# Kernel optimization log

Hardware: AMD Instinct MI355X
Metric: run time of the kernel (lower is better)

The kernel has to match this reference:

```python
import math
import jax, jax.numpy as jnp
import numpy as np

FACTOR = 2  # init kwarg of AutoCorrelation


def setup_inputs() -> dict:
    key0 = jax.random.key(0)
    kq, kk, kv = jax.random.split(key0, 3)
    B, H, L, D = 8, 8, 2048, 64
    return {
        "query": jax.random.normal(kq, (B, H, L, D), dtype=jnp.float32),
        "key": jax.random.normal(kk, (B, H, L, D), dtype=jnp.float32),
        "value": jax.random.normal(kv, (B, H, L, D), dtype=jnp.float32),
    }


def reference(query, key, value):
    # Inference (eval-mode) path of AutoCorrelation.forward.
    B, H, L, D = query.shape
    L_KV = key.shape[2]
    # _pad_or_truncate_key_value: match key/value length to query length
    if L > L_KV:
        pad = [(0, 0), (0, 0), (0, L - L_KV), (0, 0)]
        key = jnp.pad(key, pad)
        value = jnp.pad(value, pad)
    else:
        key = key[:, :, :L, :]
        value = value[:, :, :L, :]

    # _period_based_dependency: circular cross-correlation via FFT
    qf = jnp.fft.rfft(jnp.swapaxes(query, -2, -1), axis=-1)   # (B,H,D,L//2+1) complex
    kf = jnp.fft.rfft(jnp.swapaxes(key, -2, -1), axis=-1)
    corr = jnp.fft.irfft(qf * jnp.conj(kf), n=L, axis=-1)     # (B,H,D,L)

    # _time_delay_aggregation (eval branch: per-batch topk delays)
    mean_corr = corr.mean(axis=(1, 2))                         # (B,L)
    num_delays = min(FACTOR * math.ceil(math.log(L)), L)
    w, delay_idx = jax.lax.top_k(mean_corr, num_delays)       # (B,k)
    w = jax.nn.softmax(w, axis=-1)

    ar = jnp.arange(L)

    def body(ctx, inp):
        d, wk = inp  # (B,), (B,)
        idx = (ar[None, :] + d[:, None]) % L                   # (B,L) — circular shift == gather from doubled value
        gathered = jnp.take_along_axis(
            value, jnp.broadcast_to(idx[:, None, :, None], value.shape), axis=2
        )                                                      # (B,H,L,D)
        return ctx + wk[:, None, None, None] * gathered, None

    ctx0 = jnp.zeros_like(value)
    context, _ = jax.lax.scan(body, ctx0, (delay_idx.T, w.T))
    return context
```

## Files before the change

### kernel.cpp

```cpp
#include <hip/hip_runtime.h>

static constexpr int LSEQ = 2048;
static constexpr int NB   = 8;
static constexpr int NH   = 8;
static constexpr int ND   = 64;
static constexpr int NDEL = 16;

static constexpr size_t WS_P_OFF     = 0;
static constexpr size_t WS_W_OFF     = 8388608;
static constexpr size_t WS_DELAY_OFF = 8389120;

__device__ __forceinline__ int SWZ(int x) { return x ^ (((x >> 4) & 7) << 1); }

__device__ __forceinline__ int pof(int f) {
    return ((f & 7) << 8) | (((f >> 3) & 7) << 5) | (((f >> 6) & 7) << 2) | (f >> 9);
}
__device__ __forceinline__ int fofp(int p) {
    return (p >> 8) | (((p >> 5) & 7) << 3) | (((p >> 2) & 7) << 6) | ((p & 3) << 9);
}

#define CMUL(ar, ai, br, bi) make_float2((ar)*(br) - (ai)*(bi), (ar)*(bi) + (ai)*(br))

__device__ __forceinline__ void dft8(const float2 x[8], float2 X[8]) {
    const float RH = 0.70710678118654752440f;
    float2 a0 = make_float2(x[0].x + x[4].x, x[0].y + x[4].y);
    float2 a1 = make_float2(x[1].x + x[5].x, x[1].y + x[5].y);
    float2 a2 = make_float2(x[2].x + x[6].x, x[2].y + x[6].y);
    float2 a3 = make_float2(x[3].x + x[7].x, x[3].y + x[7].y);
    float2 b0 = make_float2(x[0].x - x[4].x, x[0].y - x[4].y);
    float  t1r = x[1].x - x[5].x, t1i = x[1].y - x[5].y;
    float2 b1 = make_float2(RH * (t1r + t1i), RH * (t1i - t1r));
    float  t2r = x[2].x - x[6].x, t2i = x[2].y - x[6].y;
    float2 b2 = make_float2(t2i, -t2r);
    float  t3r = x[3].x - x[7].x, t3i = x[3].y - x[7].y;
    float2 b3 = make_float2(RH * (t3i - t3r), -RH * (t3r + t3i));
    float2 c0 = make_float2(a0.x + a2.x, a0.y + a2.y);
    float2 d0 = make_float2(a0.x - a2.x, a0.y - a2.y);
    float2 c1 = make_float2(a1.x + a3.x, a1.y + a3.y);
    float2 d1 = make_float2(a1.y - a3.y, -(a1.x - a3.x));
    X[0] = make_float2(c0.x + c1.x, c0.y + c1.y);
    X[4] = make_float2(c0.x - c1.x, c0.y - c1.y);
    X[2] = make_float2(d0.x + d1.x, d0.y + d1.y);
    X[6] = make_float2(d0.x - d1.x, d0.y - d1.y);
    float2 e0 = make_float2(b0.x + b2.x, b0.y + b2.y);
    float2 f0 = make_float2(b0.x - b2.x, b0.y - b2.y);
    float2 e1 = make_float2(b1.x + b3.x, b1.y + b3.y);
    float2 f1 = make_float2(b1.y - b3.y, -(b1.x - b3.x));
    X[1] = make_float2(e0.x + e1.x, e0.y + e1.y);
    X[5] = make_float2(e0.x - e1.x, e0.y - e1.y);
    X[3] = make_float2(f0.x + f1.x, f0.y + f1.y);
    X[7] = make_float2(f0.x - f1.x, f0.y - f1.y);
}

__device__ __forceinline__ void dft4(const float2 x[4], float2 X[4]) {
    float2 s0 = make_float2(x[0].x + x[2].x, x[0].y + x[2].y);
    float2 s1 = make_float2(x[1].x + x[3].x, x[1].y + x[3].y);
    float2 d0 = make_float2(x[0].x - x[2].x, x[0].y - x[2].y);
    float2 d1 = make_float2(x[1].y - x[3].y, -(x[1].x - x[3].x));
    X[0] = make_float2(s0.x + s1.x, s0.y + s1.y);
    X[2] = make_float2(s0.x - s1.x, s0.y - s1.y);
    X[1] = make_float2(d0.x + d1.x, d0.y + d1.y);
    X[3] = make_float2(d0.x - d1.x, d0.y - d1.y);
}

__device__ __forceinline__ void stageR8(float2* zp, const int adr[8], const float2 W[7]) {
    float2 X[8], Y[8];
    #pragma unroll
    for (int j = 0; j < 8; ++j) X[j] = zp[adr[j]];
    dft8(X, Y);
    #pragma unroll
    for (int m = 1; m < 8; ++m) Y[m] = CMUL(Y[m].x, Y[m].y, W[m-1].x, W[m-1].y);
    #pragma unroll
    for (int m = 0; m < 8; ++m) zp[adr[m]] = Y[m];
}

__device__ __forceinline__ void stageD(float2* zp, const int adr[8], float2 X[8]) {
    float2 xin[8];
    #pragma unroll
    for (int j = 0; j < 8; ++j) xin[j] = zp[adr[j]];
    dft4(&xin[0], &X[0]);
    dft4(&xin[4], &X[4]);
    #pragma unroll
    for (int m = 0; m < 8; ++m) zp[adr[m]] = X[m];
}

__global__ __launch_bounds__(256, 2) void fft_corr(const float* __restrict__ q,
                                                   const float* __restrict__ k,
                                                   float2* __restrict__ Pc) {
    __shared__ float2 z0[LSEQ], z1[LSEQ];
    const int t    = threadIdx.x;
    const int bi   = blockIdx.x;
    const int xcd  = bi & 7;
    const int sl   = bi >> 3;
    const int bh   = xcd * 8 + (sl >> 4);
    const int grp  = (sl >> 1) & 7;
    const int half = sl & 1;
    const int b    = bh >> 3;
    const int h    = bh & 7;
    const size_t base = (size_t)bh * LSEQ * ND + (size_t)(grp * 8 + half * 4);

    float2 WA[7], WB[7], WC[7];
    {
        float sn, cs;
        __sincosf(-6.28318530717958647692f * (float)t / 2048.f, &sn, &cs);
        WA[0] = make_float2(cs, sn);
        __sincosf(-6.28318530717958647692f * (float)(t & 31) / 256.f, &sn, &cs);
        WB[0] = make_float2(cs, sn);
        __sincosf(-6.28318530717958647692f * (float)(t & 3) / 32.f, &sn, &cs);
        WC[0] = make_float2(cs, sn);
        #pragma unroll
        for (int m = 1; m < 7; ++m) {
            WA[m] = CMUL(WA[m-1].x, WA[m-1].y, WA[0].x, WA[0].y);
            WB[m] = CMUL(WB[m-1].x, WB[m-1].y, WB[0].x, WB[0].y);
            WC[m] = CMUL(WC[m-1].x, WC[m-1].y, WC[0].x, WC[0].y);
        }
    }

    int fS[4], pmS[4];
    #pragma unroll
    for (int s = 0; s < 4; ++s) {
        const int cc = (s < 2) ? s : s + 2;
        const int f  = fofp(8 * t + cc);
        const int m  = (2048 - f) & 2047;
        fS[s]  = f;
        pmS[s] = SWZ(pof(m));
    }
    float aFr[4] = {0, 0, 0, 0}, aFi[4] = {0, 0, 0, 0};
    float aS = 0.f;

    const int sbB   = (t >> 5) * 256 + (t & 31);
    const int baseC = (t >> 2) * 32 + (t & 3);
    int adrB[8], adrC[8], adrD[8];
    #pragma unroll
    for (int n = 0; n < 8; ++n) {
        adrB[n] = SWZ(sbB + 32 * n);
        adrC[n] = SWZ(baseC + 4 * n);
        adrD[n] = SWZ(8 * t + n);
    }

    float4 qa[8], ka[8];
    #pragma unroll
    for (int j = 0; j < 8; ++j) {
        const size_t r = base + (size_t)(t + 256 * j) * ND;
        qa[j] = *(const float4*)(q + r);
        ka[j] = *(const float4*)(k + r);
    }
    #pragma unroll
    for (int pr = 0; pr < 2; ++pr) {
        const int c0 = 2 * pr, c1 = 2 * pr + 1;
        float2 X0[8], X1[8], Y0[8], Y1[8];
        #pragma unroll
        for (int j = 0; j < 8; ++j) {
            X0[j] = make_float2((&qa[j].x)[c0], (&ka[j].x)[c0]);
            X1[j] = make_float2((&qa[j].x)[c1], (&ka[j].x)[c1]);
        }
        __syncthreads();

        dft8(X0, Y0);
        dft8(X1, Y1);
        #pragma unroll
        for (int m = 1; m < 8; ++m) {
            Y0[m] = CMUL(Y0[m].x, Y0[m].y, WA[m-1].x, WA[m-1].y);
            Y1[m] = CMUL(Y1[m].x, Y1[m].y, WA[m-1].x, WA[m-1].y);
        }
        #pragma unroll
        for (int m = 0; m < 8; ++m) {
            const int a = SWZ(m * 256 + t);
            z0[a] = Y0[m];
            z1[a] = Y1[m];
        }
        __syncthreads();

        stageR8(z0, adrB, WB);
        stageR8(z1, adrB, WB);
        __syncthreads();

        stageR8(z0, adrC, WC);
        stageR8(z1, adrC, WC);
        __syncthreads();

        stageD(z0, adrD, X0);
        stageD(z1, adrD, X1);
        __syncthreads();

        #pragma unroll
        for (int s = 0; s < 4; ++s) {
            const int cc = (s < 2) ? s : s + 2;
            {
                const float2 Zf = X0[cc], Zm = z0[pmS[s]];
                const float qr = 0.5f * (Zf.x + Zm.x), qi = 0.5f * (Zf.y - Zm.y);
                const float kr = 0.5f * (Zf.y + Zm.y), ki = 0.5f * (Zm.x - Zf.x);
                aFr[s] += qr * kr + qi * ki;
                aFi[s] += qi * kr - qr * ki;
            }
            {
                const float2 Zf = X1[cc], Zm = z1[pmS[s]];
                const float qr = 0.5f * (Zf.x + Zm.x), qi = 0.5f * (Zf.y - Zm.y);
                const float kr = 0.5f * (Zf.y + Zm.y), ki = 0.5f * (Zm.x - Zf.x);
                aFr[s] += qr * kr + qi * ki;
                aFi[s] += qi * kr - qr * ki;
            }
        }
        if (t == 0) aS += X0[2].x * X0[2].y + X1[2].x * X1[2].y;
    }

    const int part = h * 16 + grp * 2 + half;
    float2* Pp = Pc + (size_t)part * (NB * 1024) + (size_t)b * 1024;
    #pragma unroll
    for (int s = 0; s < 4; ++s) Pp[fS[s]] = make_float2(aFr[s], aFi[s]);
    if (t == 0) Pp[0] = make_float2(aFr[0], aS);
}

__global__ __launch_bounds__(256) void reduce_S(float2* __restrict__ Pc) {
    const int g = blockIdx.x * 256 + threadIdx.x;
    float ax = 0.f, ay = 0.f;
    #pragma unroll 8
    for (int part = 0; part < 128; ++part) {
        const float2 v = Pc[(size_t)part * (NB * 1024) + g];
        ax += v.x; ay += v.y;
    }
    Pc[g] = make_float2(ax, ay);
}

__global__ __launch_bounds__(256) void ifft_topk(const float2* __restrict__ S,
                                                 float* __restrict__ wout,
                                                 int* __restrict__ dout) {
    __shared__ float2 zz[LSEQ];
    __shared__ float  mc[LSEQ];
    __shared__ float  pv[4];
    __shared__ int    pig[4];
    __shared__ float  topv[NDEL];
    __shared__ int    topi[NDEL];
    const int b = blockIdx.x, t = threadIdx.x;

    float2 WA[7], WB[7], WC[7];
    {
        float sn, cs;
        __sincosf(-6.28318530717958647692f * (float)t / 2048.f, &sn, &cs);
        WA[0] = make_float2(cs, sn);
        __sincosf(-6.28318530717958647692f * (float)(t & 31) / 256.f, &sn, &cs);
        WB[0] = make_float2(cs, sn);
        __sincosf(-6.28318530717958647692f * (float)(t & 3) / 32.f, &sn, &cs);
        WC[0] = make_float2(cs, sn);
        #pragma unroll
        for (int m = 1; m < 7; ++m) {
            WA[m] = CMUL(WA[m-1].x, WA[m-1].y, WA[0].x, WA[0].y);
            WB[m] = CMUL(WB[m-1].x, WB[m-1].y, WB[0].x, WB[0].y);
            WC[m] = CMUL(WC[m-1].x, WC[m-1].y, WC[0].x, WC[0].y);
        }
    }
    const int sbB   = (t >> 5) * 256 + (t & 31);
    const int baseC = (t >> 2) * 32 + (t & 3);
    int adrB[8], adrC[8], adrD[8];
    #pragma unroll
    for (int n = 0; n < 8; ++n) {
        adrB[n] = SWZ(sbB + 32 * n);
        adrC[n] = SWZ(baseC + 4 * n);
        adrD[n] = SWZ(8 * t + n);
    }

    #pragma unroll
    for (int u = 0; u < 4; ++u) {
        const int j = t + 256 * u;
        const float2 s = S[b * 1024 + j];
        if (j == 0) {
            zz[0] = make_float2(s.x, 0.f);
            zz[2] = make_float2(s.y, 0.f);
        } else {
            zz[pof(j)]        = s;
            zz[pof(2048 - j)] = make_float2(s.x, -s.y);
        }
    }
    __syncthreads();

    float2 X[8], Y[8];
    #pragma unroll
    for (int j = 0; j < 8; ++j) {
        const float2 s = zz[pof(t + 256 * j)];
        X[j] = make_float2(s.x, -s.y);
    }
    __syncthreads();

    dft8(X, Y);
    #pragma unroll
    for (int m = 1; m < 8; ++m) Y[m] = CMUL(Y[m].x, Y[m].y, WA[m-1].x, WA[m-1].y);
    #pragma unroll
    for (int m = 0; m < 8; ++m) zz[SWZ(m * 256 + t)] = Y[m];
    __syncthreads();

    stageR8(zz, adrB, WB);
    __syncthreads();
    stageR8(zz, adrC, WC);
    __syncthreads();

    {
        float2 xin[8];
        #pragma unroll
        for (int j = 0; j < 8; ++j) xin[j] = zz[adrD[j]];
        dft4(&xin[0], &X[0]);
        dft4(&xin[4], &X[4]);
    }

    const float scale = 1.0f / ((float)LSEQ * (float)(NH * ND));
    #pragma unroll
    for (int cc = 0; cc < 8; ++cc) mc[fofp(8 * t + cc)] = X[cc].x * scale;
    __syncthreads();

    const int lane = t & 63, wv = t >> 6;
    for (int it = 0; it < NDEL; ++it) {
        float bv = -3e38f; int bix = 0;
        #pragma unroll
        for (int u = 0; u < 8; ++u) {
            const int idx = t + 256 * u;
            const float v = mc[idx];
            if (v > bv || (v == bv && idx < bix)) { bv = v; bix = idx; }
        }
        #pragma unroll
        for (int off = 32; off; off >>= 1) {
            const float ov = __shfl_xor(bv, off);
            const int   oi = __shfl_xor(bix, off);
            if (ov > bv || (ov == bv && oi < bix)) { bv = ov; bix = oi; }
        }
        if (lane == 0) { pv[wv] = bv; pig[wv] = bix; }
        __syncthreads();
        if (t < 64) {
            float v = (t < 4) ? pv[t] : -3e38f;
            int  ii = (t < 4) ? pig[t] : 0;
            #pragma unroll
            for (int off = 2; off; off >>= 1) {
                const float ov = __shfl_xor(v, off);
                const int   oi = __shfl_xor(ii, off);
                if (ov > v || (ov == v && oi < ii)) { v = ov; ii = oi; }
            }
            if (t == 0) { topv[it] = v; topi[it] = ii; mc[ii] = -3e38f; }
        }
        __syncthreads();
    }

    if (t == 0) {
        const float m = topv[0];
        float e[NDEL], sum = 0.f;
        for (int i = 0; i < NDEL; ++i) { e[i] = __expf(topv[i] - m); sum += e[i]; }
        const float inv = 1.0f / sum;
        for (int i = 0; i < NDEL; ++i) {
            wout[b * NDEL + i] = e[i] * inv;
            dout[b * NDEL + i] = topi[i];
        }
    }
}

__global__ __launch_bounds__(256) void gather_out(const float* __restrict__ v,
                                                  const float* __restrict__ w,
                                                  const int* __restrict__ delay,
                                                  float* __restrict__ out) {
    const int bi  = blockIdx.x;
    const int xcd = bi & 7;
    const int s   = bi >> 3;
    const int bh  = xcd * 8 + (s >> 7);
    const int bt  = s & 127;
    const int b   = bh >> 3;
    const int tid = threadIdx.x;

    __shared__ float sw_[NDEL];
    __shared__ int   sd_[NDEL];
    if (tid < NDEL) {
        sw_[tid] = w[b * NDEL + tid];
        sd_[tid] = delay[b * NDEL + tid];
    }
    __syncthreads();

    const float* vb = v + (size_t)bh * LSEQ * ND;
    float*       ob = out + (size_t)bh * LSEQ * ND;

    const int row = tid >> 4;
    const int col = (tid & 15) * 4;
    const int t   = bt * 16 + row;

    float4 acc = make_float4(0.f, 0.f, 0.f, 0.f);
    #pragma unroll
    for (int kk = 0; kk < NDEL; ++kk) {
        const int r = (t + sd_[kk]) & (LSEQ - 1);
        const float4 vv = *(const float4*)(vb + (size_t)r * ND + col);
        const float wv = sw_[kk];
        acc.x += wv * vv.x; acc.y += wv * vv.y;
        acc.z += wv * vv.z; acc.w += wv * vv.w;
    }
    *(float4*)(ob + (size_t)t * ND + col) = acc;
}

extern "C" void kernel_launch(void* const* d_in, const int* in_sizes, int n_in,
                              void* d_out, int out_size, void* d_ws, size_t ws_size,
                              hipStream_t stream) {
    const float* q = (const float*)d_in[0];
    const float* k = (const float*)d_in[1];
    const float* v = (const float*)d_in[2];
    float* out = (float*)d_out;

    float2* Pc    = (float2*)((char*)d_ws + WS_P_OFF);
    float*  w     = (float*)((char*)d_ws + WS_W_OFF);
    int*    delay = (int*)((char*)d_ws + WS_DELAY_OFF);

    fft_corr<<<dim3(1024), dim3(256), 0, stream>>>(q, k, Pc);
    reduce_S<<<dim3(32), dim3(256), 0, stream>>>(Pc);
    ifft_topk<<<dim3(NB), dim3(256), 0, stream>>>(Pc, w, delay);
    gather_out<<<dim3(NB * NH * 128), dim3(256), 0, stream>>>(v, w, delay, out);
}
```

Measured before the change: 209.4 us.

## Rewrite FFT correlation as per-wave register FFT with shuffle stages

```diff
diff --git a/kernel.cpp b/kernel.cpp
--- a/kernel.cpp
+++ b/kernel.cpp
@@ -20,6 +20,184 @@
 }
 
 #define CMUL(ar, ai, br, bi) make_float2((ar)*(br) - (ai)*(bi), (ar)*(bi) + (ai)*(br))
+
+__device__ __forceinline__ float2 cmulf(float2 a, float2 b) {
+    return make_float2(a.x * b.x - a.y * b.y, a.x * b.y + a.y * b.x);
+}
+
+__device__ __forceinline__ constexpr int BR5(int x) {
+    return ((x & 1) << 4) | ((x & 2) << 2) | (x & 4) | ((x & 8) >> 2) | ((x & 16) >> 4);
+}
+
+__device__ __forceinline__ void fft32_dif(float2 z[32]) {
+    constexpr float WR[16] = {
+        1.f,           0.980785280f,  0.923879533f,  0.831469612f,
+        0.707106781f,  0.555570233f,  0.382683432f,  0.195090322f,
+        0.f,          -0.195090322f, -0.382683432f, -0.555570233f,
+       -0.707106781f, -0.831469612f, -0.923879533f, -0.980785280f };
+    constexpr float WI[16] = {
+       -0.f,          -0.195090322f, -0.382683432f, -0.555570233f,
+       -0.707106781f, -0.831469612f, -0.923879533f, -0.980785280f,
+       -1.f,          -0.980785280f, -0.923879533f, -0.831469612f,
+       -0.707106781f, -0.555570233f, -0.382683432f, -0.195090322f };
+    #pragma unroll
+    for (int s = 0; s < 5; ++s) {
+        const int hh = 16 >> s;
+        #pragma unroll
+        for (int b0 = 0; b0 < 32; b0 += 2 * hh) {
+            #pragma unroll
+            for (int u = 0; u < hh; ++u) {
+                const float2 a = z[b0 + u], bb = z[b0 + u + hh];
+                z[b0 + u] = make_float2(a.x + bb.x, a.y + bb.y);
+                const float dx = a.x - bb.x, dy = a.y - bb.y;
+                const int ti = u << s;
+                z[b0 + u + hh] = (ti == 0) ? make_float2(dx, dy)
+                    : make_float2(dx * WR[ti] - dy * WI[ti],
+                                  dx * WI[ti] + dy * WR[ti]);
+            }
+        }
+    }
+}
+
+__device__ __forceinline__ float2 corrprod(float2 Zf, float2 Zm) {
+    const float qr = 0.5f * (Zf.x + Zm.x), qi = 0.5f * (Zf.y - Zm.y);
+    const float kr = 0.5f * (Zf.y + Zm.y), ki = 0.5f * (Zm.x - Zf.x);
+    return make_float2(qr * kr + qi * ki, qi * kr - qr * ki);
+}
+
+__global__ __launch_bounds__(256, 2) void fft_corr(const float* __restrict__ q,
+                                                   const float* __restrict__ k,
+                                                   float2* __restrict__ Pc) {
+    __shared__ float2 lds[4096];
+    const int t  = threadIdx.x;
+    const int w  = t >> 6;
+    const int L  = t & 63;
+    const int bi = blockIdx.x;
+    const int xcd  = bi & 7;
+    const int sl   = bi >> 3;
+    const int bh   = xcd * 8 + (sl >> 4);
+    const int dgrp = sl & 15;
+    const int b    = bh >> 3;
+    const int h    = bh & 7;
+    const size_t base = (size_t)bh * (LSEQ * ND) + (size_t)(dgrp * 4);
+
+    float2 z[32];
+
+    #pragma unroll
+    for (int P = 0; P < 2; ++P) {
+        float4 q4[4], k4[4];
+        #pragma unroll
+        for (int u = 0; u < 4; ++u) {
+            const int n = P * 1024 + t + 256 * u;
+            const size_t r = base + (size_t)n * ND;
+            q4[u] = *(const float4*)(q + r);
+            k4[u] = *(const float4*)(k + r);
+        }
+        if (P) __syncthreads();
+        #pragma unroll
+        for (int u = 0; u < 4; ++u) {
+            const int nn = t + 256 * u;
+            #pragma unroll
+            for (int c = 0; c < 4; ++c)
+                lds[c * 1024 + nn] = make_float2((&q4[u].x)[c], (&k4[u].x)[c]);
+        }
+        __syncthreads();
+        #pragma unroll
+        for (int jj = 0; jj < 16; ++jj)
+            z[16 * P + jj] = lds[w * 1024 + 64 * jj + L];
+    }
+    __syncthreads();
+
+    fft32_dif(z);
+
+    {
+        float sn, cs;
+        __sincosf(-6.28318530717958647692f * (float)L / 2048.f, &sn, &cs);
+        const float2 W1 = make_float2(cs, sn);
+        float2 Wc = W1;
+        z[BR5(1)] = cmulf(z[BR5(1)], Wc);
+        #pragma unroll
+        for (int m = 2; m < 32; ++m) {
+            Wc = cmulf(Wc, W1);
+            z[BR5(m)] = cmulf(z[BR5(m)], Wc);
+        }
+    }
+
+    #pragma unroll
+    for (int s = 0; s < 6; ++s) {
+        const int hh = 32 >> s;
+        float ts, tc;
+        __sincosf(-6.28318530717958647692f * (float)(L & (hh - 1)) /
+                      (float)(64 >> s), &ts, &tc);
+        const bool bot = (L & hh) != 0;
+        #pragma unroll
+        for (int p = 0; p < 32; ++p) {
+            const float ex = __shfl_xor(z[p].x, hh);
+            const float ey = __shfl_xor(z[p].y, hh);
+            const float ax = z[p].x + ex, ay = z[p].y + ey;
+            const float sx = ex - z[p].x, sy = ey - z[p].y;
+            const float bx = sx * tc - sy * ts;
+            const float by = sx * ts + sy * tc;
+            z[p].x = bot ? bx : ax;
+            z[p].y = bot ? by : ay;
+        }
+    }
+
+    const int kk2 = (int)(__brev((unsigned)L) >> 26);
+    const bool own = (L & 1) == 0;
+    {
+        const int mlane = (int)(__brev((unsigned)((64 - kk2) & 63)) >> 26);
+        const float zmx = __shfl(z[0].x, mlane);
+        const float zmy = __shfl(z[0].y, mlane);
+        float2 c = corrprod(z[0], make_float2(zmx, zmy));
+        const float c1024 = __shfl(c.x, 1);
+        if (L == 0) c.y = c1024;
+        if (own) lds[w * 1024 + ((kk2 << 5) | kk2)] = c;
+    }
+    #pragma unroll
+    for (int p = 1; p < 32; ++p) {
+        const int k1 = BR5(p);
+        const int pm = BR5(32 - k1);
+        const float zmx = __shfl_xor(z[pm].x, 63);
+        const float zmy = __shfl_xor(z[pm].y, 63);
+        const float2 c = corrprod(z[p], make_float2(zmx, zmy));
+        if (own) lds[w * 1024 + ((kk2 << 5) | (k1 ^ kk2))] = c;
+    }
+    __syncthreads();
+
+    float2* Pp = Pc + (size_t)(h * 16 + dgrp) * (NB * 1024) + (size_t)b * 1024;
+    #pragma unroll
+    for (int u = 0; u < 4; ++u) {
+        const int sidx = t + 256 * u;
+        const int sw = (sidx & ~31) | ((sidx & 31) ^ ((sidx >> 5) & 31));
+        float ax = 0.f, ay = 0.f;
+        #pragma unroll
+        for (int w4 = 0; w4 < 4; ++w4) {
+            const float2 v = lds[w4 * 1024 + sw];
+            ax += v.x; ay += v.y;
+        }
+        Pp[sidx] = make_float2(ax, ay);
+    }
+}
+
+__global__ __launch_bounds__(256) void reduce_S(float2* __restrict__ Pc) {
+    __shared__ float2 acc[256];
+    const int t     = threadIdx.x;
+    const int col   = blockIdx.x * 64 + (t & 63);
+    const int slice = t >> 6;
+    float ax = 0.f, ay = 0.f;
+    #pragma unroll 8
+    for (int pp = 0; pp < 32; ++pp) {
+        const float2 v = Pc[(size_t)(slice * 32 + pp) * (NB * 1024) + col];
+        ax += v.x; ay += v.y;
+    }
+    acc[t] = make_float2(ax, ay);
+    __syncthreads();
+    if (t < 64) {
+        const float2 r0 = acc[t], r1 = acc[t + 64], r2 = acc[t + 128], r3 = acc[t + 192];
+        Pc[col] = make_float2(r0.x + r1.x + r2.x + r3.x, r0.y + r1.y + r2.y + r3.y);
+    }
+}
 
 __device__ __forceinline__ void dft8(const float2 x[8], float2 X[8]) {
     const float RH = 0.70710678118654752440f;
@@ -74,154 +252,6 @@
     for (int m = 0; m < 8; ++m) zp[adr[m]] = Y[m];
 }
 
-__device__ __forceinline__ void stageD(float2* zp, const int adr[8], float2 X[8]) {
-    float2 xin[8];
-    #pragma unroll
-    for (int j = 0; j < 8; ++j) xin[j] = zp[adr[j]];
-    dft4(&xin[0], &X[0]);
-    dft4(&xin[4], &X[4]);
-    #pragma unroll
-    for (int m = 0; m < 8; ++m) zp[adr[m]] = X[m];
-}
-
-__global__ __launch_bounds__(256, 2) void fft_corr(const float* __restrict__ q,
-                                                   const float* __restrict__ k,
-                                                   float2* __restrict__ Pc) {
-    __shared__ float2 z0[LSEQ], z1[LSEQ];
-    const int t    = threadIdx.x;
-    const int bi   = blockIdx.x;
-    const int xcd  = bi & 7;
-    const int sl   = bi >> 3;
-    const int bh   = xcd * 8 + (sl >> 4);
-    const int grp  = (sl >> 1) & 7;
-    const int half = sl & 1;
-    const int b    = bh >> 3;
-    const int h    = bh & 7;
-    const size_t base = (size_t)bh * LSEQ * ND + (size_t)(grp * 8 + half * 4);
-
-    float2 WA[7], WB[7], WC[7];
-    {
-        float sn, cs;
-        __sincosf(-6.28318530717958647692f * (float)t / 2048.f, &sn, &cs);
-        WA[0] = make_float2(cs, sn);
-        __sincosf(-6.28318530717958647692f * (float)(t & 31) / 256.f, &sn, &cs);
-        WB[0] = make_float2(cs, sn);
-        __sincosf(-6.28318530717958647692f * (float)(t & 3) / 32.f, &sn, &cs);
-        WC[0] = make_float2(cs, sn);
-        #pragma unroll
-        for (int m = 1; m < 7; ++m) {
-            WA[m] = CMUL(WA[m-1].x, WA[m-1].y, WA[0].x, WA[0].y);
-            WB[m] = CMUL(WB[m-1].x, WB[m-1].y, WB[0].x, WB[0].y);
-            WC[m] = CMUL(WC[m-1].x, WC[m-1].y, WC[0].x, WC[0].y);
-        }
-    }
-
-    int fS[4], pmS[4];
-    #pragma unroll
-    for (int s = 0; s < 4; ++s) {
-        const int cc = (s < 2) ? s : s + 2;
-        const int f  = fofp(8 * t + cc);
-        const int m  = (2048 - f) & 2047;
-        fS[s]  = f;
-        pmS[s] = SWZ(pof(m));
-    }
-    float aFr[4] = {0, 0, 0, 0}, aFi[4] = {0, 0, 0, 0};
-    float aS = 0.f;
-
-    const int sbB   = (t >> 5) * 256 + (t & 31);
-    const int baseC = (t >> 2) * 32 + (t & 3);
-    int adrB[8], adrC[8], adrD[8];
-    #pragma unroll
-    for (int n = 0; n < 8; ++n) {
-        adrB[n] = SWZ(sbB + 32 * n);
-        adrC[n] = SWZ(baseC + 4 * n);
-        adrD[n] = SWZ(8 * t + n);
-    }
-
-    float4 qa[8], ka[8];
-    #pragma unroll
-    for (int j = 0; j < 8; ++j) {
-        const size_t r = base + (size_t)(t + 256 * j) * ND;
-        qa[j] = *(const float4*)(q + r);
-        ka[j] = *(const float4*)(k + r);
-    }
-    #pragma unroll
-    for (int pr = 0; pr < 2; ++pr) {
-        const int c0 = 2 * pr, c1 = 2 * pr + 1;
-        float2 X0[8], X1[8], Y0[8], Y1[8];
-        #pragma unroll
-        for (int j = 0; j < 8; ++j) {
-            X0[j] = make_float2((&qa[j].x)[c0], (&ka[j].x)[c0]);
-            X1[j] = make_float2((&qa[j].x)[c1], (&ka[j].x)[c1]);
-        }
-        __syncthreads();
-
-        dft8(X0, Y0);
-        dft8(X1, Y1);
-        #pragma unroll
-        for (int m = 1; m < 8; ++m) {
-            Y0[m] = CMUL(Y0[m].x, Y0[m].y, WA[m-1].x, WA[m-1].y);
-            Y1[m] = CMUL(Y1[m].x, Y1[m].y, WA[m-1].x, WA[m-1].y);
-        }
-        #pragma unroll
-        for (int m = 0; m < 8; ++m) {
-            const int a = SWZ(m * 256 + t);
-            z0[a] = Y0[m];
-            z1[a] = Y1[m];
-        }
-        __syncthreads();
-
-        stageR8(z0, adrB, WB);
-        stageR8(z1, adrB, WB);
-        __syncthreads();
-
-        stageR8(z0, adrC, WC);
-        stageR8(z1, adrC, WC);
-        __syncthreads();
-
-        stageD(z0, adrD, X0);
-        stageD(z1, adrD, X1);
-        __syncthreads();
-
-        #pragma unroll
-        for (int s = 0; s < 4; ++s) {
-            const int cc = (s < 2) ? s : s + 2;
-            {
-                const float2 Zf = X0[cc], Zm = z0[pmS[s]];
-                const float qr = 0.5f * (Zf.x + Zm.x), qi = 0.5f * (Zf.y - Zm.y);
-                const float kr = 0.5f * (Zf.y + Zm.y), ki = 0.5f * (Zm.x - Zf.x);
-                aFr[s] += qr * kr + qi * ki;
-                aFi[s] += qi * kr - qr * ki;
-            }
-            {
-                const float2 Zf = X1[cc], Zm = z1[pmS[s]];
-                const float qr = 0.5f * (Zf.x + Zm.x), qi = 0.5f * (Zf.y - Zm.y);
-                const float kr = 0.5f * (Zf.y + Zm.y), ki = 0.5f * (Zm.x - Zf.x);
-                aFr[s] += qr * kr + qi * ki;
-                aFi[s] += qi * kr - qr * ki;
-            }
-        }
-        if (t == 0) aS += X0[2].x * X0[2].y + X1[2].x * X1[2].y;
-    }
-
-    const int part = h * 16 + grp * 2 + half;
-    float2* Pp = Pc + (size_t)part * (NB * 1024) + (size_t)b * 1024;
-    #pragma unroll
-    for (int s = 0; s < 4; ++s) Pp[fS[s]] = make_float2(aFr[s], aFi[s]);
-    if (t == 0) Pp[0] = make_float2(aFr[0], aS);
-}
-
-__global__ __launch_bounds__(256) void reduce_S(float2* __restrict__ Pc) {
-    const int g = blockIdx.x * 256 + threadIdx.x;
-    float ax = 0.f, ay = 0.f;
-    #pragma unroll 8
-    for (int part = 0; part < 128; ++part) {
-        const float2 v = Pc[(size_t)part * (NB * 1024) + g];
-        ax += v.x; ay += v.y;
-    }
-    Pc[g] = make_float2(ax, ay);
-}
-
 __global__ __launch_bounds__(256) void ifft_topk(const float2* __restrict__ S,
                                                  float* __restrict__ wout,
                                                  int* __restrict__ dout) {
@@ -401,7 +431,7 @@
     int*    delay = (int*)((char*)d_ws + WS_DELAY_OFF);
 
     fft_corr<<<dim3(1024), dim3(256), 0, stream>>>(q, k, Pc);
-    reduce_S<<<dim3(32), dim3(256), 0, stream>>>(Pc);
+    reduce_S<<<dim3(128), dim3(256), 0, stream>>>(Pc);
     ifft_topk<<<dim3(NB), dim3(256), 0, stream>>>(Pc, w, delay);
     gather_out<<<dim3(NB * NH * 128), dim3(256), 0, stream>>>(v, w, delay, out);
 }
```

New measurement: 212.8 us. Within noise of the previous version (+1.6%).

## Rewrite inverse FFT/top-k as single-wavefront register FFT; split reduction across more blocks

Applied to the files above, without the earlier changes.

```diff
diff --git a/kernel.cpp b/kernel.cpp
--- a/kernel.cpp
+++ b/kernel.cpp
@@ -20,6 +20,44 @@
 }
 
 #define CMUL(ar, ai, br, bi) make_float2((ar)*(br) - (ai)*(bi), (ar)*(bi) + (ai)*(br))
+
+__device__ __forceinline__ float2 cmulf(float2 a, float2 b) {
+    return make_float2(a.x * b.x - a.y * b.y, a.x * b.y + a.y * b.x);
+}
+
+__device__ __forceinline__ constexpr int BR5(int x) {
+    return ((x & 1) << 4) | ((x & 2) << 2) | (x & 4) | ((x & 8) >> 2) | ((x & 16) >> 4);
+}
+
+__device__ __forceinline__ void fft32_dif(float2 z[32]) {
+    constexpr float WR[16] = {
+        1.f,           0.980785280f,  0.923879533f,  0.831469612f,
+        0.707106781f,  0.555570233f,  0.382683432f,  0.195090322f,
+        0.f,          -0.195090322f, -0.382683432f, -0.555570233f,
+       -0.707106781f, -0.831469612f, -0.923879533f, -0.980785280f };
+    constexpr float WI[16] = {
+       -0.f,          -0.195090322f, -0.382683432f, -0.555570233f,
+       -0.707106781f, -0.831469612f, -0.923879533f, -0.980785280f,
+       -1.f,          -0.980785280f, -0.923879533f, -0.831469612f,
+       -0.707106781f, -0.555570233f, -0.382683432f, -0.195090322f };
+    #pragma unroll
+    for (int s = 0; s < 5; ++s) {
+        const int hh = 16 >> s;
+        #pragma unroll
+        for (int b0 = 0; b0 < 32; b0 += 2 * hh) {
+            #pragma unroll
+            for (int u = 0; u < hh; ++u) {
+                const float2 a = z[b0 + u], bb = z[b0 + u + hh];
+                z[b0 + u] = make_float2(a.x + bb.x, a.y + bb.y);
+                const float dx = a.x - bb.x, dy = a.y - bb.y;
+                const int ti = u << s;
+                z[b0 + u + hh] = (ti == 0) ? make_float2(dx, dy)
+                    : make_float2(dx * WR[ti] - dy * WI[ti],
+                                  dx * WI[ti] + dy * WR[ti]);
+            }
+        }
+    }
+}
 
 __device__ __forceinline__ void dft8(const float2 x[8], float2 X[8]) {
     const float RH = 0.70710678118654752440f;
@@ -212,136 +250,114 @@
 }
 
 __global__ __launch_bounds__(256) void reduce_S(float2* __restrict__ Pc) {
-    const int g = blockIdx.x * 256 + threadIdx.x;
+    __shared__ float2 acc[256];
+    const int t     = threadIdx.x;
+    const int col   = blockIdx.x * 64 + (t & 63);
+    const int slice = t >> 6;
     float ax = 0.f, ay = 0.f;
     #pragma unroll 8
-    for (int part = 0; part < 128; ++part) {
-        const float2 v = Pc[(size_t)part * (NB * 1024) + g];
+    for (int pp = 0; pp < 32; ++pp) {
+        const float2 v = Pc[(size_t)(slice * 32 + pp) * (NB * 1024) + col];
         ax += v.x; ay += v.y;
     }
-    Pc[g] = make_float2(ax, ay);
-}
-
-__global__ __launch_bounds__(256) void ifft_topk(const float2* __restrict__ S,
-                                                 float* __restrict__ wout,
-                                                 int* __restrict__ dout) {
-    __shared__ float2 zz[LSEQ];
-    __shared__ float  mc[LSEQ];
-    __shared__ float  pv[4];
-    __shared__ int    pig[4];
-    __shared__ float  topv[NDEL];
-    __shared__ int    topi[NDEL];
-    const int b = blockIdx.x, t = threadIdx.x;
-
-    float2 WA[7], WB[7], WC[7];
+    acc[t] = make_float2(ax, ay);
+    __syncthreads();
+    if (t < 64) {
+        const float2 r0 = acc[t], r1 = acc[t + 64], r2 = acc[t + 128], r3 = acc[t + 192];
+        Pc[col] = make_float2(r0.x + r1.x + r2.x + r3.x, r0.y + r1.y + r2.y + r3.y);
+    }
+}
+
+__global__ __launch_bounds__(64) void ifft_topk(const float2* __restrict__ S,
+                                                float* __restrict__ wout,
+                                                int* __restrict__ dout) {
+    const int b = blockIdx.x;
+    const int L = threadIdx.x;
+    const int k2 = (int)(__brev((unsigned)L) >> 26);
+    const int base32 = k2 << 5;
+
+    float2 z[32];
+    #pragma unroll
+    for (int j = 0; j < 32; ++j) {
+        const int f   = 64 * j + L;
+        const int idx = (f < 1024) ? f : ((f == 1024) ? 0 : 2048 - f);
+        const float2 s = S[b * 1024 + idx];
+        float2 x;
+        if (f == 0)         x = make_float2(s.x, 0.f);
+        else if (f == 1024) x = make_float2(s.y, 0.f);
+        else if (f < 1024)  x = make_float2(s.x, -s.y);
+        else                x = make_float2(s.x,  s.y);
+        z[j] = x;
+    }
+
+    fft32_dif(z);
+
     {
         float sn, cs;
-        __sincosf(-6.28318530717958647692f * (float)t / 2048.f, &sn, &cs);
-        WA[0] = make_float2(cs, sn);
-        __sincosf(-6.28318530717958647692f * (float)(t & 31) / 256.f, &sn, &cs);
-        WB[0] = make_float2(cs, sn);
-        __sincosf(-6.28318530717958647692f * (float)(t & 3) / 32.f, &sn, &cs);
-        WC[0] = make_float2(cs, sn);
-        #pragma unroll
-        for (int m = 1; m < 7; ++m) {
-            WA[m] = CMUL(WA[m-1].x, WA[m-1].y, WA[0].x, WA[0].y);
-            WB[m] = CMUL(WB[m-1].x, WB[m-1].y, WB[0].x, WB[0].y);
-            WC[m] = CMUL(WC[m-1].x, WC[m-1].y, WC[0].x, WC[0].y);
-        }
-    }
-    const int sbB   = (t >> 5) * 256 + (t & 31);
-    const int baseC = (t >> 2) * 32 + (t & 3);
-    int adrB[8], adrC[8], adrD[8];
-    #pragma unroll
-    for (int n = 0; n < 8; ++n) {
-        adrB[n] = SWZ(sbB + 32 * n);
-        adrC[n] = SWZ(baseC + 4 * n);
-        adrD[n] = SWZ(8 * t + n);
-    }
-
-    #pragma unroll
-    for (int u = 0; u < 4; ++u) {
-        const int j = t + 256 * u;
-        const float2 s = S[b * 1024 + j];
-        if (j == 0) {
-            zz[0] = make_float2(s.x, 0.f);
-            zz[2] = make_float2(s.y, 0.f);
-        } else {
-            zz[pof(j)]        = s;
-            zz[pof(2048 - j)] = make_float2(s.x, -s.y);
-        }
-    }
-    __syncthreads();
-
-    float2 X[8], Y[8];
-    #pragma unroll
-    for (int j = 0; j < 8; ++j) {
-        const float2 s = zz[pof(t + 256 * j)];
-        X[j] = make_float2(s.x, -s.y);
-    }
-    __syncthreads();
-
-    dft8(X, Y);
-    #pragma unroll
-    for (int m = 1; m < 8; ++m) Y[m] = CMUL(Y[m].x, Y[m].y, WA[m-1].x, WA[m-1].y);
-    #pragma unroll
-    for (int m = 0; m < 8; ++m) zz[SWZ(m * 256 + t)] = Y[m];
-    __syncthreads();
-
-    stageR8(zz, adrB, WB);
-    __syncthreads();
-    stageR8(zz, adrC, WC);
-    __syncthreads();
-
-    {
-        float2 xin[8];
-        #pragma unroll
-        for (int j = 0; j < 8; ++j) xin[j] = zz[adrD[j]];
-        dft4(&xin[0], &X[0]);
-        dft4(&xin[4], &X[4]);
+        __sincosf(-6.28318530717958647692f * (float)L / 2048.f, &sn, &cs);
+        const float2 W1 = make_float2(cs, sn);
+        float2 Wc = W1;
+        z[BR5(1)] = cmulf(z[BR5(1)], Wc);
+        #pragma unroll
+        for (int m = 2; m < 32; ++m) {
+            Wc = cmulf(Wc, W1);
+            z[BR5(m)] = cmulf(z[BR5(m)], Wc);
+        }
+    }
+
+    #pragma unroll
+    for (int s = 0; s < 6; ++s) {
+        const int hh = 32 >> s;
+        float ts, tc;
+        __sincosf(-6.28318530717958647692f * (float)(L & (hh - 1)) /
+                      (float)(64 >> s), &ts, &tc);
+        const bool bot = (L & hh) != 0;
+        #pragma unroll
+        for (int p = 0; p < 32; ++p) {
+            const float ex = __shfl_xor(z[p].x, hh);
+            const float ey = __shfl_xor(z[p].y, hh);
+            const float ax = z[p].x + ex, ay = z[p].y + ey;
+            const float sx = ex - z[p].x, sy = ey - z[p].y;
+            const float bx = sx * tc - sy * ts;
+            const float by = sx * ts + sy * tc;
+            z[p].x = bot ? bx : ax;
+            z[p].y = bot ? by : ay;
+        }
     }
 
     const float scale = 1.0f / ((float)LSEQ * (float)(NH * ND));
-    #pragma unroll
-    for (int cc = 0; cc < 8; ++cc) mc[fofp(8 * t + cc)] = X[cc].x * scale;
-    __syncthreads();
-
-    const int lane = t & 63, wv = t >> 6;
+    float vals[32];
+    #pragma unroll
+    for (int p = 0; p < 32; ++p) vals[p] = z[p].x * scale;
+
+    float topv[NDEL]; int topi[NDEL];
+    #pragma unroll
     for (int it = 0; it < NDEL; ++it) {
-        float bv = -3e38f; int bix = 0;
-        #pragma unroll
-        for (int u = 0; u < 8; ++u) {
-            const int idx = t + 256 * u;
-            const float v = mc[idx];
-            if (v > bv || (v == bv && idx < bix)) { bv = v; bix = idx; }
+        float bv = -3e38f; int btau = 1 << 30;
+        #pragma unroll
+        for (int p = 0; p < 32; ++p) {
+            const int tau = BR5(p) + base32;
+            if (vals[p] > bv || (vals[p] == bv && tau < btau)) { bv = vals[p]; btau = tau; }
         }
         #pragma unroll
         for (int off = 32; off; off >>= 1) {
             const float ov = __shfl_xor(bv, off);
-            const int   oi = __shfl_xor(bix, off);
-            if (ov > bv || (ov == bv && oi < bix)) { bv = ov; bix = oi; }
-        }
-        if (lane == 0) { pv[wv] = bv; pig[wv] = bix; }
-        __syncthreads();
-        if (t < 64) {
-            float v = (t < 4) ? pv[t] : -3e38f;
-            int  ii = (t < 4) ? pig[t] : 0;
-            #pragma unroll
-            for (int off = 2; off; off >>= 1) {
-                const float ov = __shfl_xor(v, off);
-                const int   oi = __shfl_xor(ii, off);
-                if (ov > v || (ov == v && oi < ii)) { v = ov; ii = oi; }
-            }
-            if (t == 0) { topv[it] = v; topi[it] = ii; mc[ii] = -3e38f; }
-        }
-        __syncthreads();
-    }
-
-    if (t == 0) {
+            const int   ot = __shfl_xor(btau, off);
+            if (ov > bv || (ov == bv && ot < btau)) { bv = ov; btau = ot; }
+        }
+        topv[it] = bv; topi[it] = btau;
+        #pragma unroll
+        for (int p = 0; p < 32; ++p)
+            if (BR5(p) + base32 == btau) vals[p] = -3e38f;
+    }
+
+    if (L == 0) {
         const float m = topv[0];
         float e[NDEL], sum = 0.f;
+        #pragma unroll
         for (int i = 0; i < NDEL; ++i) { e[i] = __expf(topv[i] - m); sum += e[i]; }
         const float inv = 1.0f / sum;
+        #pragma unroll
         for (int i = 0; i < NDEL; ++i) {
             wout[b * NDEL + i] = e[i] * inv;
             dout[b * NDEL + i] = topi[i];
@@ -401,7 +417,7 @@
     int*    delay = (int*)((char*)d_ws + WS_DELAY_OFF);
 
     fft_corr<<<dim3(1024), dim3(256), 0, stream>>>(q, k, Pc);
-    reduce_S<<<dim3(32), dim3(256), 0, stream>>>(Pc);
-    ifft_topk<<<dim3(NB), dim3(256), 0, stream>>>(Pc, w, delay);
+    reduce_S<<<dim3(128), dim3(256), 0, stream>>>(Pc);
+    ifft_topk<<<dim3(NB), dim3(64), 0, stream>>>(Pc, w, delay);
     gather_out<<<dim3(NB * NH * 128), dim3(256), 0, stream>>>(v, w, delay, out);
 }
```

New measurement: 226.3 us. +8.0%, slower.
